# Performance work log

Measured on AMD Instinct MI355X. Metric: run time of the kernel, lower is better.

The kernel has to match this reference:

```python
import jax, jax.numpy as jnp
import numpy as np

B, S, D_IN, D_OUT, H = 2, 2048, 1024, 1024, 16
DK = D_OUT // H


def setup_inputs() -> dict:
    key = jax.random.key(0)
    ks = jax.random.split(key, 6)
    s_in = 1.0 / np.sqrt(D_IN)
    s_out = 1.0 / np.sqrt(D_OUT)
    return {
        "x": jax.random.normal(ks[0], (B, S, D_IN), dtype=jnp.float32),
        "Wq": jax.random.uniform(ks[1], (D_OUT, D_IN), jnp.float32, -s_in, s_in),
        "Wk": jax.random.uniform(ks[2], (D_OUT, D_IN), jnp.float32, -s_in, s_in),
        "Wv": jax.random.uniform(ks[3], (D_OUT, D_IN), jnp.float32, -s_in, s_in),
        "Wo": jax.random.uniform(ks[4], (D_OUT, D_OUT), jnp.float32, -s_out, s_out),
        "bo": jax.random.uniform(ks[5], (D_OUT,), jnp.float32, -s_out, s_out),
    }


def reference(x, Wq, Wk, Wv, Wo, bo):
    b, s, _ = x.shape
    # torch Linear: y = x @ W.T
    q = (x @ Wq.T).reshape(b, s, H, DK).transpose(0, 2, 1, 3)  # [b,h,s,dk]
    k = (x @ Wk.T).reshape(b, s, H, DK).transpose(0, 2, 1, 3)
    v = (x @ Wv.T).reshape(b, s, H, DK).transpose(0, 2, 1, 3)
    scores = jnp.einsum("bhqd,bhkd->bhqk", q, k)
    causal = jnp.tril(jnp.ones((s, s), dtype=bool))  # True = keep
    scores = jnp.where(causal, scores, -jnp.inf)
    attn = jax.nn.softmax(scores / np.sqrt(DK), axis=-1)
    # dropout p=0.0 (eval) -> identity
    ctx = jnp.einsum("bhqk,bhkd->bhqd", attn, v)
    ctx = ctx.transpose(0, 2, 1, 3).reshape(b, s, D_OUT)
    return ctx @ Wo.T + bo
```

## Files before the change

kernel.cpp:

```cpp
#include <hip/hip_runtime.h>
#include <stdint.h>

#define B_   2
#define S_   2048
#define DIN  1024
#define DOUT 1024
#define H_   16
#define DK_  64
#define MSZ  (B_ * S_)

typedef __bf16 bf16v8 __attribute__((ext_vector_type(8)));
typedef float  f32x4  __attribute__((ext_vector_type(4)));

__device__ __forceinline__ ushort f2b(float f) {
  union { float f; uint32_t u; } a; a.f = f;
  uint32_t u = a.u;
  u += 0x7FFFu + ((u >> 16) & 1u);
  return (ushort)(u >> 16);
}

__device__ __forceinline__ uint32_t pk2(float lo, float hi) {
  union { __bf16 h; ushort u; } a, b;
  a.h = (__bf16)lo; b.h = (__bf16)hi;
  return (uint32_t)a.u | ((uint32_t)b.u << 16);
}

#define GLDS(gp, lp) __builtin_amdgcn_global_load_lds(                         \
    (const __attribute__((address_space(1))) void*)(gp),                       \
    (__attribute__((address_space(3))) void*)(lp), 16, 0, 0)

__global__ void cvt_all(const float* __restrict__ x,  const float* __restrict__ wq,
                        const float* __restrict__ wk, const float* __restrict__ wv,
                        const float* __restrict__ wo,
                        ushort* __restrict__ xb,  ushort* __restrict__ wqb,
                        ushort* __restrict__ wkb, ushort* __restrict__ wvb,
                        ushort* __restrict__ wob) {
  int i = blockIdx.x * blockDim.x + threadIdx.x;
  const int NX = 1 << 20, NW = 1 << 18;
  const float* src; ushort* dst; int off;
  if (i < NX)               { src = x;  dst = xb;  off = i; }
  else if (i < NX + NW)     { src = wq; dst = wqb; off = i - NX; }
  else if (i < NX + 2 * NW) { src = wk; dst = wkb; off = i - NX - NW; }
  else if (i < NX + 3 * NW) { src = wv; dst = wvb; off = i - NX - 2 * NW; }
  else                      { src = wo; dst = wob; off = i - NX - 3 * NW; }
  float4 v = reinterpret_cast<const float4*>(src)[off];
  ushort4 o;
  o.x = f2b(v.x); o.y = f2b(v.y); o.z = f2b(v.z); o.w = f2b(v.w);
  reinterpret_cast<ushort4*>(dst)[off] = o;
}

template<int MODE>
__global__ __launch_bounds__(256)
void gemm_nt(const ushort* __restrict__ A,
             const ushort* __restrict__ Bq, const ushort* __restrict__ Bk,
             const ushort* __restrict__ Bv,
             ushort* __restrict__ Oq, ushort* __restrict__ Ok,
             ushort* __restrict__ Vt,
             float* __restrict__ Cf, const float* __restrict__ bias,
             int M, int N, int K) {
  __shared__ ushort sA[128 * 32];
  __shared__ ushort sB[128 * 32];

  const int tid  = threadIdx.x;
  const int lane = tid & 63, wid = tid >> 6;
  const int wr = wid >> 1, wc = wid & 1;
  const int g = lane >> 4, c = lane & 15;
  const int m0 = blockIdx.x * 128, n0 = blockIdx.y * 128;

  const ushort* Bm = Bq;
  ushort* Ob = nullptr;
  float oscale = 1.0f;
  bool tv = false;
  if (MODE == 0) {
    int z = blockIdx.z;
    Bm = (z == 0) ? Bq : (z == 1) ? Bk : Bv;
    Ob = (z == 0) ? Oq : Ok;
    tv = (z == 2);
    if (z == 0) oscale = 0.125f * 1.4426950408889634f;
  }

  f32x4 acc[4][4] = {};

  for (int k0 = 0; k0 < K; k0 += 32) {
    __syncthreads();
#pragma unroll
    for (int i = 0; i < 2; ++i) {
      int o   = (i * 256 + tid) * 16;
      int row = o >> 6;
      int cb  = o & 63;
      const ushort* ga = A  + (size_t)(m0 + row) * K + k0 + (cb >> 1);
      GLDS(ga, (char*)sA + o);
      const ushort* gb = Bm + (size_t)(n0 + row) * K + k0 + (cb >> 1);
      GLDS(gb, (char*)sB + o);
    }
    __syncthreads();

    bf16v8 aF[4], bF[4];
#pragma unroll
    for (int m = 0; m < 4; ++m)
      aF[m] = *reinterpret_cast<const bf16v8*>(&sA[(wr * 64 + m * 16 + c) * 32 + g * 8]);
#pragma unroll
    for (int n = 0; n < 4; ++n)
      bF[n] = *reinterpret_cast<const bf16v8*>(&sB[(wc * 64 + n * 16 + c) * 32 + g * 8]);
#pragma unroll
    for (int m = 0; m < 4; ++m)
#pragma unroll
      for (int n = 0; n < 4; ++n)
        acc[m][n] = __builtin_amdgcn_mfma_f32_16x16x32_bf16(aF[m], bF[n], acc[m][n], 0, 0, 0);
  }

  const int rbase = m0 + wr * 64 + g * 4;
  const int cbase = n0 + wc * 64 + c;
#pragma unroll
  for (int m = 0; m < 4; ++m) {
#pragma unroll
    for (int n = 0; n < 4; ++n) {
      int col = cbase + n * 16;
      if (MODE == 1) {
        float bv = bias[col];
#pragma unroll
        for (int i = 0; i < 4; ++i)
          Cf[(size_t)(rbase + m * 16 + i) * N + col] = acc[m][n][i] + bv;
      } else if (tv) {
        int row0 = rbase + m * 16;
        int bb = row0 >> 11, ss = row0 & 2047;
        int hh = col >> 6, dd = col & 63;
        ushort4 o4;
        o4.x = f2b(acc[m][n][0]); o4.y = f2b(acc[m][n][1]);
        o4.z = f2b(acc[m][n][2]); o4.w = f2b(acc[m][n][3]);
        *reinterpret_cast<ushort4*>(
            &Vt[((size_t)(bb * 16 + hh) * 64 + dd) * 2048 + ss]) = o4;
      } else {
#pragma unroll
        for (int i = 0; i < 4; ++i)
          Ob[(size_t)(rbase + m * 16 + i) * N + col] = f2b(acc[m][n][i] * oscale);
      }
    }
  }
}

__global__ __launch_bounds__(256)
void flash_attn(const ushort* __restrict__ Q, const ushort* __restrict__ K,
                const ushort* __restrict__ Vt, ushort* __restrict__ O) {
  __shared__ ushort sK[2][64][64];
  __shared__ ushort sV[2][64][64];
  __shared__ ushort sP[4][16][64];

  const int tid  = threadIdx.x;
  const int lane = tid & 63, wid = tid >> 6;
  const int g = lane >> 4, c = lane & 15;

  const int orig = blockIdx.x;
  const int xcd  = orig & 7, d = orig >> 3;
  int qt, hoff;
  if (d < 64) { qt = 31 - (d >> 1); hoff = d & 1; }
  else        { int e = d - 64; qt = e >> 1; hoff = 2 + (e & 1); }
  const int bh = xcd * 4 + hoff;
  const int b = bh >> 4, h = bh & 15;
  const int q0 = qt * 64;

  const ushort* Qb = Q  + (size_t)b * S_ * DOUT + h * DK_;
  const ushort* Kb = K  + (size_t)b * S_ * DOUT + h * DK_;
  const ushort* Vb = Vt + (size_t)bh * DK_ * S_;

  const int sr   = lane >> 3;
  const int swc  = ((lane & 7) ^ sr) << 3;
  const int row0 = wid * 8 + sr;
  const int msk  = (c & 7) << 4;
  const int pswz = (c & 7) << 2;

  bf16v8 qf[2];
  {
    const ushort* qrow = Qb + (size_t)(q0 + wid * 16 + c) * DOUT;
    qf[0] = *reinterpret_cast<const bf16v8*>(qrow + g * 8);
    qf[1] = *reinterpret_cast<const bf16v8*>(qrow + 32 + g * 8);
  }

  bf16v8 ones;
#pragma unroll
  for (int j = 0; j < 8; ++j) ones[j] = (__bf16)1.0f;

#pragma unroll
  for (int j = 0; j < 2; ++j) {
    int r = j * 32 + row0;
    GLDS(Kb + (size_t)r * DOUT + swc,
         (char*)&sK[0][0][0] + (j * 32 + wid * 8) * 128 + lane * 16);
    GLDS(Vb + (size_t)r * S_ + swc,
         (char*)&sV[0][0][0] + (j * 32 + wid * 8) * 128 + lane * 16);
  }
  __syncthreads();

  f32x4 accO[4] = {};
  f32x4 accL = {};
  char* sPw = (char*)&sP[wid][0][0];
  const int qg = q0 + wid * 16 + c;
  const int qdiag = q0 + wid * 16;

  int buf = 0;
  for (int kv0 = 0; kv0 <= q0; kv0 += 64, buf ^= 1) {
    if (kv0 + 64 <= q0) {
      const int nb = buf ^ 1, kvn = kv0 + 64;
#pragma unroll
      for (int j = 0; j < 2; ++j) {
        int r = j * 32 + row0;
        GLDS(Kb + (size_t)(kvn + r) * DOUT + swc,
             (char*)&sK[nb][0][0] + (j * 32 + wid * 8) * 128 + lane * 16);
        GLDS(Vb + (size_t)r * S_ + kvn + swc,
             (char*)&sV[nb][0][0] + (j * 32 + wid * 8) * 128 + lane * 16);
      }
    }

    const char* cK = (const char*)&sK[buf][0][0];
    const char* cV = (const char*)&sV[buf][0][0];

    f32x4 s[4] = {};
    __builtin_amdgcn_s_setprio(1);
#pragma unroll
    for (int nf = 0; nf < 4; ++nf) {
      const char* rp = cK + (nf * 16 + c) * 128;
#pragma unroll
      for (int ks = 0; ks < 2; ++ks) {
        bf16v8 kf = *reinterpret_cast<const bf16v8*>(rp + ((ks * 64 + g * 16) ^ msk));
        s[nf] = __builtin_amdgcn_mfma_f32_16x16x32_bf16(kf, qf[ks], s[nf], 0, 0, 0);
      }
    }
    __builtin_amdgcn_s_setprio(0);

    if (kv0 + 63 > qdiag) {
#pragma unroll
      for (int nf = 0; nf < 4; ++nf)
#pragma unroll
        for (int i = 0; i < 4; ++i)
          if (kv0 + nf * 16 + g * 4 + i > qg) s[nf][i] = -1e30f;
    }

#pragma unroll
    for (int nf = 0; nf < 4; ++nf) {
      float p0 = exp2f(s[nf][0]), p1 = exp2f(s[nf][1]);
      float p2 = exp2f(s[nf][2]), p3 = exp2f(s[nf][3]);
      uint2 w2; w2.x = pk2(p0, p1); w2.y = pk2(p2, p3);
      *reinterpret_cast<uint2*>(
          sPw + c * 128 + (((nf * 8 + g * 2) ^ pswz) << 2)) = w2;
    }
    bf16v8 pf[2];
#pragma unroll
    for (int ks = 0; ks < 2; ++ks)
      pf[ks] = *reinterpret_cast<const bf16v8*>(
          sPw + c * 128 + (((ks * 16 + g * 4) ^ pswz) << 2));

    __builtin_amdgcn_s_setprio(1);
#pragma unroll
    for (int ks = 0; ks < 2; ++ks)
      accL = __builtin_amdgcn_mfma_f32_16x16x32_bf16(pf[ks], ones, accL, 0, 0, 0);
#pragma unroll
    for (int nf2 = 0; nf2 < 4; ++nf2) {
      const char* vp = cV + (nf2 * 16 + c) * 128;
#pragma unroll
      for (int ks = 0; ks < 2; ++ks) {
        bf16v8 vf = *reinterpret_cast<const bf16v8*>(vp + ((ks * 64 + g * 16) ^ msk));
        accO[nf2] = __builtin_amdgcn_mfma_f32_16x16x32_bf16(pf[ks], vf, accO[nf2], 0, 0, 0);
      }
    }
    __builtin_amdgcn_s_setprio(0);

    __syncthreads();
  }

#pragma unroll
  for (int nf = 0; nf < 4; ++nf)
#pragma unroll
    for (int i = 0; i < 4; ++i) {
      int prow = g * 4 + i;
      float v = accO[nf][i] / accL[i];
      *(ushort*)(sPw + prow * 128 +
                 ((nf * 32 + c * 2) ^ ((prow & 7) << 4))) = f2b(v);
    }
  {
    const int r = lane >> 2, cq = lane & 3;
    const char* base = sPw + r * 128;
    const int m2 = (r & 7) << 4;
    bf16v8 t0 = *reinterpret_cast<const bf16v8*>(base + ((cq * 32) ^ m2));
    bf16v8 t1 = *reinterpret_cast<const bf16v8*>(base + ((cq * 32 + 16) ^ m2));
    ushort* Gb = O + (size_t)b * S_ * DOUT +
                 (size_t)(q0 + wid * 16 + r) * DOUT + h * DK_ + cq * 16;
    *reinterpret_cast<bf16v8*>(Gb) = t0;
    *reinterpret_cast<bf16v8*>(Gb + 8) = t1;
  }
}

extern "C" void kernel_launch(void* const* d_in, const int* in_sizes, int n_in,
                              void* d_out, int out_size, void* d_ws, size_t ws_size,
                              hipStream_t stream) {
  const float* x  = (const float*)d_in[0];
  const float* Wq = (const float*)d_in[1];
  const float* Wk = (const float*)d_in[2];
  const float* Wv = (const float*)d_in[3];
  const float* Wo = (const float*)d_in[4];
  const float* bo = (const float*)d_in[5];
  float* out = (float*)d_out;

  char* ws = (char*)d_ws;
  const size_t MB = (size_t)1 << 20;
  ushort* xb  = (ushort*)(ws);
  ushort* wqb = (ushort*)(ws +  8 * MB);
  ushort* wkb = (ushort*)(ws + 10 * MB);
  ushort* wvb = (ushort*)(ws + 12 * MB);
  ushort* wob = (ushort*)(ws + 14 * MB);
  ushort* qb  = (ushort*)(ws + 16 * MB);
  ushort* kb  = (ushort*)(ws + 24 * MB);
  ushort* vtb = (ushort*)(ws + 32 * MB);
  ushort* cb  = (ushort*)(ws);

  const int ncv = (1 << 20) + 4 * (1 << 18);
  cvt_all<<<ncv / 256, 256, 0, stream>>>(x, Wq, Wk, Wv, Wo,
                                         xb, wqb, wkb, wvb, wob);

  dim3 gqkv(MSZ / 128, DOUT / 128, 3);
  gemm_nt<0><<<gqkv, 256, 0, stream>>>(xb, wqb, wkb, wvb, qb, kb, vtb,
                                       nullptr, nullptr, MSZ, DOUT, DIN);

  flash_attn<<<B_ * H_ * (S_ / 64), 256, 0, stream>>>(qb, kb, vtb, cb);

  dim3 gproj(MSZ / 128, DOUT / 128, 1);
  gemm_nt<1><<<gproj, 256, 0, stream>>>(cb, wob, nullptr, nullptr,
                                        nullptr, nullptr, nullptr, out, bo,
                                        MSZ, DOUT, DOUT);
}
```

Baseline: 126.2 us.

## Pair complementary causal query tiles in one 512-thread flash-attention block

Each flash-attention block now has 8 waves covering two query tiles, tp and 31-tp. The two tiles share the K/V tiles staged in LDS, and every block gets the same causal work. This halves the grid, removes the earlier scheduling scheme that reordered tiles by length, and cuts K/V global loads in half. In exchange, the short-tile waves sit idle at barriers for the rest of the long tile's loop, and the larger blocks may reduce occupancy.

```diff
diff --git a/kernel.cpp b/kernel.cpp
--- a/kernel.cpp
+++ b/kernel.cpp
@@ -139,39 +139,38 @@
   }
 }
 
-__global__ __launch_bounds__(256)
+__global__ __launch_bounds__(512)
 void flash_attn(const ushort* __restrict__ Q, const ushort* __restrict__ K,
                 const ushort* __restrict__ Vt, ushort* __restrict__ O) {
   __shared__ ushort sK[2][64][64];
   __shared__ ushort sV[2][64][64];
-  __shared__ ushort sP[4][16][64];
+  __shared__ ushort sP[8][16][64];
 
   const int tid  = threadIdx.x;
   const int lane = tid & 63, wid = tid >> 6;
+  const int wid4 = wid & 3;
   const int g = lane >> 4, c = lane & 15;
 
   const int orig = blockIdx.x;
-  const int xcd  = orig & 7, d = orig >> 3;
-  int qt, hoff;
-  if (d < 64) { qt = 31 - (d >> 1); hoff = d & 1; }
-  else        { int e = d - 64; qt = e >> 1; hoff = 2 + (e & 1); }
-  const int bh = xcd * 4 + hoff;
+  const int xcd  = orig & 7, idc = orig >> 3;
+  const int bh   = xcd * 4 + (idc >> 4);
+  const int tp   = idc & 15;
   const int b = bh >> 4, h = bh & 15;
-  const int q0 = qt * 64;
+  const int q0    = (wid < 4) ? tp * 64 : (31 - tp) * 64;
+  const int q0max = (31 - tp) * 64;
 
   const ushort* Qb = Q  + (size_t)b * S_ * DOUT + h * DK_;
   const ushort* Kb = K  + (size_t)b * S_ * DOUT + h * DK_;
   const ushort* Vb = Vt + (size_t)bh * DK_ * S_;
 
-  const int sr   = lane >> 3;
-  const int swc  = ((lane & 7) ^ sr) << 3;
-  const int row0 = wid * 8 + sr;
+  const int srow = tid >> 3;
+  const int swc  = ((tid & 7) ^ (srow & 7)) << 3;
   const int msk  = (c & 7) << 4;
   const int pswz = (c & 7) << 2;
 
   bf16v8 qf[2];
   {
-    const ushort* qrow = Qb + (size_t)(q0 + wid * 16 + c) * DOUT;
+    const ushort* qrow = Qb + (size_t)(q0 + wid4 * 16 + c) * DOUT;
     qf[0] = *reinterpret_cast<const bf16v8*>(qrow + g * 8);
     qf[1] = *reinterpret_cast<const bf16v8*>(qrow + 32 + g * 8);
   }
@@ -180,88 +179,80 @@
 #pragma unroll
   for (int j = 0; j < 8; ++j) ones[j] = (__bf16)1.0f;
 
-#pragma unroll
-  for (int j = 0; j < 2; ++j) {
-    int r = j * 32 + row0;
-    GLDS(Kb + (size_t)r * DOUT + swc,
-         (char*)&sK[0][0][0] + (j * 32 + wid * 8) * 128 + lane * 16);
-    GLDS(Vb + (size_t)r * S_ + swc,
-         (char*)&sV[0][0][0] + (j * 32 + wid * 8) * 128 + lane * 16);
-  }
+  GLDS(Kb + (size_t)srow * DOUT + swc, (char*)&sK[0][0][0] + tid * 16);
+  GLDS(Vb + (size_t)srow * S_  + swc, (char*)&sV[0][0][0] + tid * 16);
   __syncthreads();
 
   f32x4 accO[4] = {};
   f32x4 accL = {};
   char* sPw = (char*)&sP[wid][0][0];
-  const int qg = q0 + wid * 16 + c;
-  const int qdiag = q0 + wid * 16;
+  const int qg = q0 + wid4 * 16 + c;
+  const int qdiag = q0 + wid4 * 16;
 
   int buf = 0;
-  for (int kv0 = 0; kv0 <= q0; kv0 += 64, buf ^= 1) {
-    if (kv0 + 64 <= q0) {
+  for (int kv0 = 0; kv0 <= q0max; kv0 += 64, buf ^= 1) {
+    if (kv0 + 64 <= q0max) {
       const int nb = buf ^ 1, kvn = kv0 + 64;
-#pragma unroll
-      for (int j = 0; j < 2; ++j) {
-        int r = j * 32 + row0;
-        GLDS(Kb + (size_t)(kvn + r) * DOUT + swc,
-             (char*)&sK[nb][0][0] + (j * 32 + wid * 8) * 128 + lane * 16);
-        GLDS(Vb + (size_t)r * S_ + kvn + swc,
-             (char*)&sV[nb][0][0] + (j * 32 + wid * 8) * 128 + lane * 16);
-      }
-    }
-
-    const char* cK = (const char*)&sK[buf][0][0];
-    const char* cV = (const char*)&sV[buf][0][0];
-
-    f32x4 s[4] = {};
-    __builtin_amdgcn_s_setprio(1);
-#pragma unroll
-    for (int nf = 0; nf < 4; ++nf) {
-      const char* rp = cK + (nf * 16 + c) * 128;
-#pragma unroll
-      for (int ks = 0; ks < 2; ++ks) {
-        bf16v8 kf = *reinterpret_cast<const bf16v8*>(rp + ((ks * 64 + g * 16) ^ msk));
-        s[nf] = __builtin_amdgcn_mfma_f32_16x16x32_bf16(kf, qf[ks], s[nf], 0, 0, 0);
-      }
-    }
-    __builtin_amdgcn_s_setprio(0);
-
-    if (kv0 + 63 > qdiag) {
-#pragma unroll
-      for (int nf = 0; nf < 4; ++nf)
-#pragma unroll
-        for (int i = 0; i < 4; ++i)
-          if (kv0 + nf * 16 + g * 4 + i > qg) s[nf][i] = -1e30f;
-    }
-
-#pragma unroll
-    for (int nf = 0; nf < 4; ++nf) {
-      float p0 = exp2f(s[nf][0]), p1 = exp2f(s[nf][1]);
-      float p2 = exp2f(s[nf][2]), p3 = exp2f(s[nf][3]);
-      uint2 w2; w2.x = pk2(p0, p1); w2.y = pk2(p2, p3);
-      *reinterpret_cast<uint2*>(
-          sPw + c * 128 + (((nf * 8 + g * 2) ^ pswz) << 2)) = w2;
-    }
-    bf16v8 pf[2];
-#pragma unroll
-    for (int ks = 0; ks < 2; ++ks)
-      pf[ks] = *reinterpret_cast<const bf16v8*>(
-          sPw + c * 128 + (((ks * 16 + g * 4) ^ pswz) << 2));
-
-    __builtin_amdgcn_s_setprio(1);
-#pragma unroll
-    for (int ks = 0; ks < 2; ++ks)
-      accL = __builtin_amdgcn_mfma_f32_16x16x32_bf16(pf[ks], ones, accL, 0, 0, 0);
-#pragma unroll
-    for (int nf2 = 0; nf2 < 4; ++nf2) {
-      const char* vp = cV + (nf2 * 16 + c) * 128;
-#pragma unroll
-      for (int ks = 0; ks < 2; ++ks) {
-        bf16v8 vf = *reinterpret_cast<const bf16v8*>(vp + ((ks * 64 + g * 16) ^ msk));
-        accO[nf2] = __builtin_amdgcn_mfma_f32_16x16x32_bf16(pf[ks], vf, accO[nf2], 0, 0, 0);
-      }
-    }
-    __builtin_amdgcn_s_setprio(0);
+      GLDS(Kb + (size_t)(kvn + srow) * DOUT + swc,
+           (char*)&sK[nb][0][0] + tid * 16);
+      GLDS(Vb + (size_t)srow * S_ + kvn + swc,
+           (char*)&sV[nb][0][0] + tid * 16);
+    }
+
+    if (kv0 <= q0) {
+      const char* cK = (const char*)&sK[buf][0][0];
+      const char* cV = (const char*)&sV[buf][0][0];
+
+      f32x4 s[4] = {};
+      __builtin_amdgcn_s_setprio(1);
+#pragma unroll
+      for (int nf = 0; nf < 4; ++nf) {
+        const char* rp = cK + (nf * 16 + c) * 128;
+#pragma unroll
+        for (int ks = 0; ks < 2; ++ks) {
+          bf16v8 kf = *reinterpret_cast<const bf16v8*>(rp + ((ks * 64 + g * 16) ^ msk));
+          s[nf] = __builtin_amdgcn_mfma_f32_16x16x32_bf16(kf, qf[ks], s[nf], 0, 0, 0);
+        }
+      }
+      __builtin_amdgcn_s_setprio(0);
+
+      if (kv0 + 63 > qdiag) {
+#pragma unroll
+        for (int nf = 0; nf < 4; ++nf)
+#pragma unroll
+          for (int i = 0; i < 4; ++i)
+            if (kv0 + nf * 16 + g * 4 + i > qg) s[nf][i] = -1e30f;
+      }
+
+#pragma unroll
+      for (int nf = 0; nf < 4; ++nf) {
+        float p0 = exp2f(s[nf][0]), p1 = exp2f(s[nf][1]);
+        float p2 = exp2f(s[nf][2]), p3 = exp2f(s[nf][3]);
+        uint2 w2; w2.x = pk2(p0, p1); w2.y = pk2(p2, p3);
+        *reinterpret_cast<uint2*>(
+            sPw + c * 128 + (((nf * 8 + g * 2) ^ pswz) << 2)) = w2;
+      }
+      bf16v8 pf[2];
+#pragma unroll
+      for (int ks = 0; ks < 2; ++ks)
+        pf[ks] = *reinterpret_cast<const bf16v8*>(
+            sPw + c * 128 + (((ks * 16 + g * 4) ^ pswz) << 2));
+
+      __builtin_amdgcn_s_setprio(1);
+#pragma unroll
+      for (int ks = 0; ks < 2; ++ks)
+        accL = __builtin_amdgcn_mfma_f32_16x16x32_bf16(pf[ks], ones, accL, 0, 0, 0);
+#pragma unroll
+      for (int nf2 = 0; nf2 < 4; ++nf2) {
+        const char* vp = cV + (nf2 * 16 + c) * 128;
+#pragma unroll
+        for (int ks = 0; ks < 2; ++ks) {
+          bf16v8 vf = *reinterpret_cast<const bf16v8*>(vp + ((ks * 64 + g * 16) ^ msk));
+          accO[nf2] = __builtin_amdgcn_mfma_f32_16x16x32_bf16(pf[ks], vf, accO[nf2], 0, 0, 0);
+        }
+      }
+      __builtin_amdgcn_s_setprio(0);
+    }
 
     __syncthreads();
   }
@@ -282,7 +273,7 @@
     bf16v8 t0 = *reinterpret_cast<const bf16v8*>(base + ((cq * 32) ^ m2));
     bf16v8 t1 = *reinterpret_cast<const bf16v8*>(base + ((cq * 32 + 16) ^ m2));
     ushort* Gb = O + (size_t)b * S_ * DOUT +
-                 (size_t)(q0 + wid * 16 + r) * DOUT + h * DK_ + cq * 16;
+                 (size_t)(q0 + wid4 * 16 + r) * DOUT + h * DK_ + cq * 16;
     *reinterpret_cast<bf16v8*>(Gb) = t0;
     *reinterpret_cast<bf16v8*>(Gb + 8) = t1;
   }
@@ -319,7 +310,7 @@
   gemm_nt<0><<<gqkv, 256, 0, stream>>>(xb, wqb, wkb, wvb, qb, kb, vtb,
                                        nullptr, nullptr, MSZ, DOUT, DIN);
 
-  flash_attn<<<B_ * H_ * (S_ / 64), 256, 0, stream>>>(qb, kb, vtb, cb);
+  flash_attn<<<B_ * H_ * (S_ / 128), 512, 0, stream>>>(qb, kb, vtb, cb);
 
   dim3 gproj(MSZ / 128, DOUT / 128, 1);
   gemm_nt<1><<<gproj, 256, 0, stream>>>(cb, wob, nullptr, nullptr,
```

Result: faster. 119.9 us (-5.0%).
